# Kernel optimization log

Hardware: AMD Instinct MI355X
Metric: run time of the kernel (lower is better)

Reference implementation:

```python
import jax, jax.numpy as jnp
import numpy as np

N = 30000      # nodes
E = 480000     # edges (no self loops; GATConv adds them)
IN = 256       # in_features
OUT = 128      # out_features == per-head channels (concat=False)
H = 4          # heads
NEG_SLOPE = 0.2


def setup_inputs() -> dict:
    key = jax.random.key(0)
    k = jax.random.split(key, 6)
    x = jax.random.normal(k[0], (N, IN), dtype=jnp.float32)
    src = jax.random.randint(k[1], (E,), 0, N, dtype=jnp.int32)
    # guarantee no self loops (GATConv would strip them before re-adding)
    off = jax.random.randint(k[2], (E,), 1, N, dtype=jnp.int32)
    dst = (src + off) % N
    edge_index = jnp.stack([src, dst])  # [2, E]
    W = jax.random.normal(k[3], (IN, H * OUT), dtype=jnp.float32) / np.float32(np.sqrt(IN))
    att_src = jax.random.normal(k[4], (H, OUT), dtype=jnp.float32) / np.float32(np.sqrt(OUT))
    att_dst = jax.random.normal(k[5], (H, OUT), dtype=jnp.float32) / np.float32(np.sqrt(OUT))
    bias = jnp.zeros((OUT,), dtype=jnp.float32)
    return {"x": x, "edge_index": edge_index, "W": W,
            "att_src": att_src, "att_dst": att_dst, "bias": bias}


def reference(x, edge_index, W, att_src, att_dst, bias):
    n = x.shape[0]
    # dense projection -> per-head features [N, H, C]
    h = (x @ W).reshape(n, H, OUT)
    a_s = jnp.einsum('nhc,hc->nh', h, att_src)  # [N, H]
    a_d = jnp.einsum('nhc,hc->nh', h, att_dst)  # [N, H]
    # add self loops (GATConv default add_self_loops=True)
    loop = jnp.arange(n, dtype=edge_index.dtype)
    src = jnp.concatenate([edge_index[0], loop])  # [Et]
    dst = jnp.concatenate([edge_index[1], loop])  # [Et]
    # per-edge attention logits + LeakyReLU
    alpha = jax.nn.leaky_relu(a_s[src] + a_d[dst], NEG_SLOPE)  # [Et, H]
    # segment softmax over incoming edges of each dst node
    amax = jax.ops.segment_max(alpha, dst, num_segments=n)      # [N, H]
    ex = jnp.exp(alpha - amax[dst])
    denom = jax.ops.segment_sum(ex, dst, num_segments=n)        # [N, H]
    w = ex / denom[dst]                                          # [Et, H]
    # gather source features, weight, scatter-add to dst
    msg = h[src] * w[:, :, None]                                 # [Et, H, C]
    out = jax.ops.segment_sum(msg, dst, num_segments=n)          # [N, H, C]
    # concat=False -> mean over heads, then bias, then module's tanh
    out = out.mean(axis=1) + bias                                # [N, C]
    return jnp.tanh(out)
```

## Files before the change

### kernel.cpp

```cpp
#include <hip/hip_runtime.h>
#include <math.h>

#define IN_F   256
#define OUT_F  128
#define HEADS  4
#define HD     (HEADS * OUT_F)
#define K2     1024
#define NEG    0.2f
#define CAP    64

typedef __attribute__((ext_vector_type(8))) short short8;
typedef __attribute__((ext_vector_type(4))) float f32x4;
typedef __attribute__((ext_vector_type(2))) float f32x2;

typedef __attribute__((address_space(1))) const void* gp_t;
typedef __attribute__((address_space(3))) void* lp_t;

static __device__ __forceinline__ ushort f2bf(float f) {
    union { float f; unsigned u; } v; v.f = f;
    unsigned r = (v.u + 0x7FFFu + ((v.u >> 16) & 1u)) >> 16;
    return (ushort)r;
}
static __device__ __forceinline__ float bflo(unsigned u) {
    union { unsigned u; float f; } v; v.u = u << 16; return v.f;
}
static __device__ __forceinline__ float bfhi(unsigned u) {
    union { unsigned u; float f; } v; v.u = u & 0xFFFF0000u; return v.f;
}

#define PKFMA(D, A, B) asm("v_pk_fma_f32 %0, %1, %2, %0" : "+v"(D) : "v"(A), "v"(B))

__global__ __launch_bounds__(256) void prep1(const float* __restrict__ W,
                                             const float* __restrict__ att_src,
                                             const float* __restrict__ att_dst,
                                             ushort* __restrict__ WT2,
                                             float* __restrict__ va_s,
                                             float* __restrict__ va_d,
                                             int* __restrict__ cursor,
                                             int n_nodes) {
    const int b = blockIdx.x;
    const int tid = threadIdx.x;
    if (b < 512) {
        int idx = b * 256 + tid;
        int cout = idx >> 10, kk = idx & 1023;
        int h = kk >> 8, c = kk & 255;
        WT2[idx] = f2bf(W[(size_t)c * HD + h * OUT_F + cout]);
    } else if (b < 768) {
        const int lane = tid & 63;
        const int p = (b - 512) * 4 + (tid >> 6);
        const int h = p >> 8;
        const int k = p & 255;
        const float* wr = W + (size_t)k * HD + h * OUT_F;
        float w0 = wr[lane], w1 = wr[lane + 64];
        float s0 = att_src[h * OUT_F + lane], s1 = att_src[h * OUT_F + lane + 64];
        float d0 = att_dst[h * OUT_F + lane], d1 = att_dst[h * OUT_F + lane + 64];
        float ss = w0 * s0 + w1 * s1;
        float sd = w0 * d0 + w1 * d1;
#pragma unroll
        for (int off = 32; off > 0; off >>= 1) {
            ss += __shfl_xor(ss, off, 64);
            sd += __shfl_xor(sd, off, 64);
        }
        if (lane == 0) { va_s[p] = ss; va_d[p] = sd; }
    } else {
        int i = (b - 768) * 256 + tid;
        if (i < n_nodes) cursor[i] = 0;
    }
}

__global__ __launch_bounds__(256) void prep2(const float* __restrict__ X,
                                             const float* __restrict__ va_s,
                                             const float* __restrict__ va_d,
                                             const int* __restrict__ src,
                                             const int* __restrict__ dst,
                                             ushort* __restrict__ Xb,
                                             float* __restrict__ a_s,
                                             float* __restrict__ a_d,
                                             int* __restrict__ cursor,
                                             int* __restrict__ table,
                                             int n_nodes, int n_edges, int nebk) {
    const int b = blockIdx.x;
    const int tid = threadIdx.x;
    if (b < nebk) {
        int e = b * 256 + tid;
        if (e < n_edges) {
            int d = dst[e];
            int r = atomicAdd(&cursor[d], 1);
            if (r < CAP) table[(size_t)d * CAP + r] = src[e];
        }
        return;
    }
    const int lane = tid & 63;
    const int node = (b - nebk) * 4 + (tid >> 6);
    if (node >= n_nodes) return;
    float4 v = *(const float4*)(X + (size_t)node * IN_F + lane * 4);
    ushort4 o; o.x = f2bf(v.x); o.y = f2bf(v.y); o.z = f2bf(v.z); o.w = f2bf(v.w);
    *(ushort4*)(Xb + (size_t)node * IN_F + lane * 4) = o;

    float ps[HEADS], pd[HEADS];
#pragma unroll
    for (int hd = 0; hd < HEADS; ++hd) {
        float4 s4 = *(const float4*)(va_s + hd * IN_F + lane * 4);
        float4 d4 = *(const float4*)(va_d + hd * IN_F + lane * 4);
        ps[hd] = v.x * s4.x + v.y * s4.y + v.z * s4.z + v.w * s4.w;
        pd[hd] = v.x * d4.x + v.y * d4.y + v.z * d4.z + v.w * d4.w;
    }
#pragma unroll
    for (int off = 32; off > 0; off >>= 1) {
#pragma unroll
        for (int hd = 0; hd < HEADS; ++hd) {
            ps[hd] += __shfl_xor(ps[hd], off, 64);
            pd[hd] += __shfl_xor(pd[hd], off, 64);
        }
    }
    if (lane == 0) {
        float4 s4 = make_float4(ps[0], ps[1], ps[2], ps[3]);
        float4 d4 = make_float4(pd[0], pd[1], pd[2], pd[3]);
        *(float4*)(a_s + node * 4) = s4;
        *(float4*)(a_d + node * 4) = d4;
    }
}

#define EDGE(E8)                                                            \
    {                                                                       \
        uint u = *(const uint*)(cons + (E8) * 256);                         \
        float4 wA = *(const float4*)(wp + (E8) * 8);                        \
        float4 wB = *(const float4*)(wp + (E8) * 8 + 4);                    \
        f32x2 f = {bflo(u), bfhi(u)};                                       \
        f32x2 w0p = {wA.x, wA.y}, w1p = {wA.z, wA.w};                       \
        f32x2 w2p = {wB.x, wB.y}, w3p = {wB.z, wB.w};                       \
        PKFMA(ah[0], f, w0p); PKFMA(ah[1], f, w1p);                         \
        PKFMA(ah[2], f, w2p); PKFMA(ah[3], f, w3p);                         \
    }

#define ISSUE(EB, DST)                                                      \
    {                                                                       \
        asm volatile("s_waitcnt lgkmcnt(0)" ::: "memory");                  \
        int ea_ = __shfl(sreg, (EB) + (lane >> 4), 64);                     \
        int eb_ = __shfl(sreg, (EB) + 4 + (lane >> 4), 64);                 \
        __builtin_amdgcn_global_load_lds((gp_t)(xb16 + (size_t)ea_ * 256),  \
                                         (lp_t)(DST), 16, 0, 0);            \
        __builtin_amdgcn_global_load_lds((gp_t)(xb16 + (size_t)eb_ * 256),  \
                                         (lp_t)((DST) + 1024), 16, 0, 0);   \
    }

__global__ __launch_bounds__(256) void gat_agg(const ushort* __restrict__ Xb,
                                               const float* __restrict__ a_s,
                                               const float* __restrict__ a_d,
                                               const int* __restrict__ cursor,
                                               const int* __restrict__ table,
                                               ushort* __restrict__ Zb,
                                               int n_nodes) {
    __shared__ ushort xst[4][2][8][128];
    __shared__ float wse[4][CAP][8];
    const int lane = threadIdx.x & 63;
    const int wid  = threadIdx.x >> 6;
    const int n = blockIdx.x * 2 + (wid >> 1);
    const int half = wid & 1;
    if (n >= n_nodes) return;
    int deg = cursor[n]; if (deg > CAP) deg = CAP;
    const int* row = table + (size_t)n * CAP;
    const bool act = lane < deg;
    int sreg = act ? row[lane] : n;

    const ushort* xb16 = Xb + half * 128 + (lane & 15) * 8;
    uint uself = *(const uint*)(Xb + (size_t)n * IN_F + half * 128 + lane * 2);

    const int ntiles = (deg + 7) >> 3;
    if (ntiles > 0) ISSUE(0, (char*)&xst[wid][0][0][0]);

    const float4 ad4 = *(const float4*)(a_d + n * 4);
    const float4 as4 = *(const float4*)(a_s + n * 4);
    const float ad[4] = {ad4.x, ad4.y, ad4.z, ad4.w};
    float aself[4];
    {
        const float asn[4] = {as4.x, as4.y, as4.z, as4.w};
#pragma unroll
        for (int hd = 0; hd < 4; ++hd) {
            float al0 = asn[hd] + ad[hd];
            aself[hd] = al0 > 0.f ? al0 : NEG * al0;
        }
    }
    float al[4];
    {
        float4 av = *(const float4*)(a_s + (size_t)sreg * 4);
        const float as_[4] = {av.x, av.y, av.z, av.w};
#pragma unroll
        for (int hd = 0; hd < 4; ++hd) {
            float a = as_[hd] + ad[hd];
            a = a > 0.f ? a : NEG * a;
            al[hd] = act ? a : -1e30f;
        }
    }
    float m[4];
#pragma unroll
    for (int hd = 0; hd < 4; ++hd) m[hd] = al[hd];
#pragma unroll
    for (int off = 32; off > 0; off >>= 1)
#pragma unroll
        for (int hd = 0; hd < 4; ++hd)
            m[hd] = fmaxf(m[hd], __shfl_xor(m[hd], off, 64));
#pragma unroll
    for (int hd = 0; hd < 4; ++hd) m[hd] = fmaxf(m[hd], aself[hd]);

    float w[4], den[4];
#pragma unroll
    for (int hd = 0; hd < 4; ++hd) {
        w[hd] = act ? __expf(al[hd] - m[hd]) : 0.f;
        den[hd] = w[hd];
    }
#pragma unroll
    for (int off = 32; off > 0; off >>= 1)
#pragma unroll
        for (int hd = 0; hd < 4; ++hd)
            den[hd] += __shfl_xor(den[hd], off, 64);

    float es[4], rdv[4];
#pragma unroll
    for (int hd = 0; hd < 4; ++hd) {
        es[hd] = __expf(aself[hd] - m[hd]);
        rdv[hd] = 1.f / (den[hd] + es[hd]);
    }

    *(float4*)&wse[wid][lane][0] = make_float4(w[0], w[0], w[1], w[1]);
    *(float4*)&wse[wid][lane][4] = make_float4(w[2], w[2], w[3], w[3]);

    f32x2 ah[4];
    {
        f32x2 s = {bflo(uself), bfhi(uself)};
#pragma unroll
        for (int hd = 0; hd < 4; ++hd) {
            f32x2 eh = {es[hd], es[hd]};
            ah[hd] = s * eh;
        }
    }
#pragma unroll 1
    for (int t = 0; t < ntiles; ++t) {
        if (t + 1 < ntiles) {
            ISSUE((t + 1) * 8, (char*)&xst[wid][(t + 1) & 1][0][0]);
            asm volatile("s_waitcnt vmcnt(2)" ::: "memory");
        } else {
            asm volatile("s_waitcnt vmcnt(0)" ::: "memory");
        }
        const char* cons = (const char*)&xst[wid][t & 1][0][0] + lane * 4;
        const float* wp = &wse[wid][t * 8][0];
        EDGE(0); EDGE(1); EDGE(2); EDGE(3);
        EDGE(4); EDGE(5); EDGE(6); EDGE(7);
    }

    ushort* zr = Zb + (size_t)n * K2 + half * 128 + lane * 2;
#pragma unroll
    for (int hd = 0; hd < 4; ++hd) {
        f32x2 r2 = {rdv[hd], rdv[hd]};
        f32x2 z = ah[hd] * r2;
        ushort2 zz; zz.x = f2bf(z.x); zz.y = f2bf(z.y);
        *(ushort2*)(zr + hd * 256) = zz;
    }
}

#define GBM 32
#define GBN 128
#define GBK 64

__global__ __launch_bounds__(256) void gemm2(const ushort* __restrict__ Zb,
                                             const ushort* __restrict__ WT2,
                                             const float* __restrict__ bias,
                                             float* __restrict__ out,
                                             int n_nodes) {
    __shared__ ushort As[2][GBM][GBK];
    __shared__ ushort Bs[2][GBN][GBK];
    const int tid = threadIdx.x;
    const int m0 = blockIdx.y * GBM;
    const int wave = tid >> 6, lane = tid & 63;
    const int wm = (wave & 1) * 16, wn = (wave >> 1) * 64;
    const int l15 = lane & 15, quad = lane >> 4;

    const int rr8 = lane >> 3;
    const int cg  = (lane & 7) ^ rr8;
    const ushort* gA0 = Zb + (size_t)(m0 + wave * 8 + rr8) * K2 + cg * 8;
    const ushort* gB0 = WT2 + (size_t)(wave * 32 + rr8) * K2 + cg * 8;
    const ushort* gB1 = gB0 + 8 * K2;
    const ushort* gB2 = gB0 + 16 * K2;
    const ushort* gB3 = gB0 + 24 * K2;

#define STAGE(T, B)                                                          \
    {                                                                        \
        const int ko_ = (T) * GBK;                                           \
        __builtin_amdgcn_global_load_lds((gp_t)(gA0 + ko_),                  \
            (lp_t)&As[B][wave * 8][0], 16, 0, 0);                            \
        __builtin_amdgcn_global_load_lds((gp_t)(gB0 + ko_),                  \
            (lp_t)&Bs[B][wave * 32][0], 16, 0, 0);                           \
        __builtin_amdgcn_global_load_lds((gp_t)(gB1 + ko_),                  \
            (lp_t)&Bs[B][wave * 32 + 8][0], 16, 0, 0);                       \
        __builtin_amdgcn_global_load_lds((gp_t)(gB2 + ko_),                  \
            (lp_t)&Bs[B][wave * 32 + 16][0], 16, 0, 0);                      \
        __builtin_amdgcn_global_load_lds((gp_t)(gB3 + ko_),                  \
            (lp_t)&Bs[B][wave * 32 + 24][0], 16, 0, 0);                      \
    }

    f32x4 acc[4];
#pragma unroll
    for (int j = 0; j < 4; ++j) acc[j] = (f32x4){0.f, 0.f, 0.f, 0.f};

    const int NT = K2 / GBK;
    STAGE(0, 0);
#pragma unroll 1
    for (int t = 0; t < NT; ++t) {
        const int b = t & 1;
        if (t + 1 < NT) {
            STAGE(t + 1, b ^ 1);
            asm volatile("s_waitcnt vmcnt(5)" ::: "memory");
        } else {
            asm volatile("s_waitcnt vmcnt(0)" ::: "memory");
        }
        asm volatile("s_barrier" ::: "memory");

#pragma unroll
        for (int tt = 0; tt < 2; ++tt) {
            const int sl = ((tt * 4 + quad) ^ (l15 & 7)) * 8;
            short8 af = *(const short8*)&As[b][wm + l15][sl];
            short8 bf_[4];
#pragma unroll
            for (int fn = 0; fn < 4; ++fn)
                bf_[fn] = *(const short8*)&Bs[b][wn + fn * 16 + l15][sl];
#pragma unroll
            for (int fn = 0; fn < 4; ++fn)
                acc[fn] = __builtin_amdgcn_mfma_f32_16x16x32_bf16(
                    af, bf_[fn], acc[fn], 0, 0, 0);
        }
        asm volatile("s_barrier" ::: "memory");
    }

    float bcol[4];
#pragma unroll
    for (int fn = 0; fn < 4; ++fn) bcol[fn] = bias[wn + fn * 16 + l15];

    int gmb = m0 + wm + quad * 4;
#pragma unroll
    for (int reg = 0; reg < 4; ++reg) {
        int gm = gmb + reg;
        if (gm < n_nodes) {
#pragma unroll
            for (int fn = 0; fn < 4; ++fn) {
                float o = tanhf(0.25f * acc[fn][reg] + bcol[fn]);
                out[(size_t)gm * OUT_F + wn + fn * 16 + l15] = o;
            }
        }
    }
}

extern "C" void kernel_launch(void* const* d_in, const int* in_sizes, int n_in,
                              void* d_out, int out_size, void* d_ws, size_t ws_size,
                              hipStream_t stream) {
    const float* x       = (const float*)d_in[0];
    const int*   ei      = (const int*)d_in[1];
    const float* W       = (const float*)d_in[2];
    const float* att_src = (const float*)d_in[3];
    const float* att_dst = (const float*)d_in[4];
    const float* bias    = (const float*)d_in[5];
    float* out = (float*)d_out;

    const int n_nodes = in_sizes[0] / IN_F;
    const int n_edges = in_sizes[1] / 2;
    const int* src = ei;
    const int* dst = ei + n_edges;

    char* ws = (char*)d_ws;
    size_t off = 0;
    auto alloc = [&](size_t bytes) -> void* {
        void* p = ws + off;
        off = (off + bytes + 255) & ~(size_t)255;
        return p;
    };
    ushort* Xb     = (ushort*)alloc((size_t)n_nodes * IN_F * sizeof(ushort));
    ushort* Zb     = (ushort*)alloc((size_t)n_nodes * K2 * sizeof(ushort));
    ushort* WT2    = (ushort*)alloc((size_t)OUT_F * K2 * sizeof(ushort));
    float*  va_s   = (float*)alloc((size_t)HEADS * IN_F * sizeof(float));
    float*  va_d   = (float*)alloc((size_t)HEADS * IN_F * sizeof(float));
    float*  a_s    = (float*)alloc((size_t)n_nodes * HEADS * sizeof(float));
    float*  a_d    = (float*)alloc((size_t)n_nodes * HEADS * sizeof(float));
    int*    cursor = (int*)alloc((size_t)n_nodes * sizeof(int));
    int*    table  = (int*)alloc((size_t)n_nodes * CAP * sizeof(int));
    (void)ws_size; (void)n_in; (void)out_size;

    const int czb  = (n_nodes + 255) / 256;
    const int nebk = (n_edges + 255) / 256;

    prep1<<<768 + czb, 256, 0, stream>>>(W, att_src, att_dst, WT2, va_s, va_d,
                                         cursor, n_nodes);
    prep2<<<nebk + (n_nodes + 3) / 4, 256, 0, stream>>>(x, va_s, va_d, src, dst,
                                                        Xb, a_s, a_d, cursor, table,
                                                        n_nodes, n_edges, nebk);
    gat_agg<<<(n_nodes + 1) / 2, 256, 0, stream>>>(Xb, a_s, a_d, cursor, table,
                                                   Zb, n_nodes);

    dim3 ggrid(1, (n_nodes + GBM - 1) / GBM);
    gemm2<<<ggrid, 256, 0, stream>>>(Zb, WT2, bias, out, n_nodes);
}
```

Before: 204.8 us.

## Fuse neighbor aggregation and output GEMM into one kernel via LDS Z tile

Merges the gat_agg and gemm2 kernels into one, so each block of 32 nodes aggregates its neighbor features into a swizzled LDS tile and then runs the bf16 MFMA projection straight from LDS. This drops the global round trip of the N x 1024 bf16 Z intermediate and one kernel launch. Each wave now handles a full 256-wide row for 8 nodes serially instead of a half row for one node, which cuts parallelism and raises LDS use (64KB Z tile plus staging). Both effects may lower occupancy and latency hiding during the irregular gather phase.

```diff
diff --git a/kernel.cpp b/kernel.cpp
--- a/kernel.cpp
+++ b/kernel.cpp
@@ -8,6 +8,9 @@
 #define K2     1024
 #define NEG    0.2f
 #define CAP    64
+#define GBN    128
+#define GBK    64
+#define NTK    (K2 / GBK)
 
 typedef __attribute__((ext_vector_type(8))) short short8;
 typedef __attribute__((ext_vector_type(4))) float f32x4;
@@ -123,193 +126,214 @@
 
 #define EDGE(E8)                                                            \
     {                                                                       \
-        uint u = *(const uint*)(cons + (E8) * 256);                         \
+        uint2 uu = *(const uint2*)(cons + (E8) * 512);                      \
         float4 wA = *(const float4*)(wp + (E8) * 8);                        \
         float4 wB = *(const float4*)(wp + (E8) * 8 + 4);                    \
-        f32x2 f = {bflo(u), bfhi(u)};                                       \
+        f32x2 f01 = {bflo(uu.x), bfhi(uu.x)};                               \
+        f32x2 f23 = {bflo(uu.y), bfhi(uu.y)};                               \
         f32x2 w0p = {wA.x, wA.y}, w1p = {wA.z, wA.w};                       \
         f32x2 w2p = {wB.x, wB.y}, w3p = {wB.z, wB.w};                       \
-        PKFMA(ah[0], f, w0p); PKFMA(ah[1], f, w1p);                         \
-        PKFMA(ah[2], f, w2p); PKFMA(ah[3], f, w3p);                         \
+        PKFMA(a01[0], f01, w0p); PKFMA(a23[0], f23, w0p);                   \
+        PKFMA(a01[1], f01, w1p); PKFMA(a23[1], f23, w1p);                   \
+        PKFMA(a01[2], f01, w2p); PKFMA(a23[2], f23, w2p);                   \
+        PKFMA(a01[3], f01, w3p); PKFMA(a23[3], f23, w3p);                   \
     }
 
 #define ISSUE(EB, DST)                                                      \
     {                                                                       \
         asm volatile("s_waitcnt lgkmcnt(0)" ::: "memory");                  \
-        int ea_ = __shfl(sreg, (EB) + (lane >> 4), 64);                     \
-        int eb_ = __shfl(sreg, (EB) + 4 + (lane >> 4), 64);                 \
-        __builtin_amdgcn_global_load_lds((gp_t)(xb16 + (size_t)ea_ * 256),  \
-                                         (lp_t)(DST), 16, 0, 0);            \
-        __builtin_amdgcn_global_load_lds((gp_t)(xb16 + (size_t)eb_ * 256),  \
-                                         (lp_t)((DST) + 1024), 16, 0, 0);   \
-    }
-
-__global__ __launch_bounds__(256) void gat_agg(const ushort* __restrict__ Xb,
-                                               const float* __restrict__ a_s,
-                                               const float* __restrict__ a_d,
-                                               const int* __restrict__ cursor,
-                                               const int* __restrict__ table,
-                                               ushort* __restrict__ Zb,
-                                               int n_nodes) {
-    __shared__ ushort xst[4][2][8][128];
+        int s0_ = __shfl(sreg, (EB) + 0, 64);                               \
+        int s1_ = __shfl(sreg, (EB) + 1, 64);                               \
+        int s2_ = __shfl(sreg, (EB) + 2, 64);                               \
+        int s3_ = __shfl(sreg, (EB) + 3, 64);                               \
+        int s4_ = __shfl(sreg, (EB) + 4, 64);                               \
+        int s5_ = __shfl(sreg, (EB) + 5, 64);                               \
+        int s6_ = __shfl(sreg, (EB) + 6, 64);                               \
+        int s7_ = __shfl(sreg, (EB) + 7, 64);                               \
+        int sa_ = (lane & 32) ? s1_ : s0_;                                  \
+        int sb_ = (lane & 32) ? s3_ : s2_;                                  \
+        int sc_ = (lane & 32) ? s5_ : s4_;                                  \
+        int sd_ = (lane & 32) ? s7_ : s6_;                                  \
+        __builtin_amdgcn_global_load_lds((gp_t)(xb16 + (size_t)sa_ * 256),  \
+                                         (lp_t)((DST) + 0 * 1024), 16, 0, 0);\
+        __builtin_amdgcn_global_load_lds((gp_t)(xb16 + (size_t)sb_ * 256),  \
+                                         (lp_t)((DST) + 1 * 1024), 16, 0, 0);\
+        __builtin_amdgcn_global_load_lds((gp_t)(xb16 + (size_t)sc_ * 256),  \
+                                         (lp_t)((DST) + 2 * 1024), 16, 0, 0);\
+        __builtin_amdgcn_global_load_lds((gp_t)(xb16 + (size_t)sd_ * 256),  \
+                                         (lp_t)((DST) + 3 * 1024), 16, 0, 0);\
+    }
+
+#define STAGEB(T, B)                                                         \
+    {                                                                        \
+        const int ko_ = (T) * GBK;                                           \
+        __builtin_amdgcn_global_load_lds((gp_t)(gB0 + ko_),                  \
+            (lp_t)&u.Bs[B][wid * 32][0], 16, 0, 0);                          \
+        __builtin_amdgcn_global_load_lds((gp_t)(gB1 + ko_),                  \
+            (lp_t)&u.Bs[B][wid * 32 + 8][0], 16, 0, 0);                      \
+        __builtin_amdgcn_global_load_lds((gp_t)(gB2 + ko_),                  \
+            (lp_t)&u.Bs[B][wid * 32 + 16][0], 16, 0, 0);                     \
+        __builtin_amdgcn_global_load_lds((gp_t)(gB3 + ko_),                  \
+            (lp_t)&u.Bs[B][wid * 32 + 24][0], 16, 0, 0);                     \
+    }
+
+union staging_u {
+    ushort xst[4][2][8][256];
+    ushort Bs[2][GBN][GBK];
+};
+
+__global__ __launch_bounds__(256) void aggemm(const ushort* __restrict__ Xb,
+                                              const float* __restrict__ a_s,
+                                              const float* __restrict__ a_d,
+                                              const int* __restrict__ cursor,
+                                              const int* __restrict__ table,
+                                              const ushort* __restrict__ WT2,
+                                              const float* __restrict__ bias,
+                                              float* __restrict__ out,
+                                              int n_nodes) {
+    __shared__ ushort Zs[32][K2];
+    __shared__ union staging_u u;
     __shared__ float wse[4][CAP][8];
+
     const int lane = threadIdx.x & 63;
     const int wid  = threadIdx.x >> 6;
-    const int n = blockIdx.x * 2 + (wid >> 1);
-    const int half = wid & 1;
-    if (n >= n_nodes) return;
-    int deg = cursor[n]; if (deg > CAP) deg = CAP;
-    const int* row = table + (size_t)n * CAP;
-    const bool act = lane < deg;
-    int sreg = act ? row[lane] : n;
-
-    const ushort* xb16 = Xb + half * 128 + (lane & 15) * 8;
-    uint uself = *(const uint*)(Xb + (size_t)n * IN_F + half * 128 + lane * 2);
-
-    const int ntiles = (deg + 7) >> 3;
-    if (ntiles > 0) ISSUE(0, (char*)&xst[wid][0][0][0]);
-
-    const float4 ad4 = *(const float4*)(a_d + n * 4);
-    const float4 as4 = *(const float4*)(a_s + n * 4);
-    const float ad[4] = {ad4.x, ad4.y, ad4.z, ad4.w};
-    float aself[4];
-    {
-        const float asn[4] = {as4.x, as4.y, as4.z, as4.w};
+    const int m0 = blockIdx.x * 32;
+
+    const ushort* xb16 = Xb + (lane & 31) * 8;
+    const uint2* xb2 = (const uint2*)Xb;
+    char* xb0 = (char*)&u.xst[wid][0][0][0];
+    char* xb1 = (char*)&u.xst[wid][1][0][0];
+
+    for (int i = 0; i < 8; ++i) {
+        const int slot = wid * 8 + i;
+        const int n = m0 + slot;
+        if (n >= n_nodes) break;
+        int deg = cursor[n]; if (deg > CAP) deg = CAP;
+        const int* row = table + (size_t)n * CAP;
+        const bool act = lane < deg;
+        int sreg = act ? row[lane] : n;
+        uint2 uself = xb2[(size_t)n * 64 + lane];
+
+        const int ntiles = (deg + 7) >> 3;
+        if (ntiles > 0) ISSUE(0, xb0);
+
+        const float4 ad4 = *(const float4*)(a_d + n * 4);
+        const float4 as4 = *(const float4*)(a_s + n * 4);
+        const float ad[4] = {ad4.x, ad4.y, ad4.z, ad4.w};
+        float aself[4];
+        {
+            const float asn[4] = {as4.x, as4.y, as4.z, as4.w};
+#pragma unroll
+            for (int hd = 0; hd < 4; ++hd) {
+                float al0 = asn[hd] + ad[hd];
+                aself[hd] = al0 > 0.f ? al0 : NEG * al0;
+            }
+        }
+        float al[4];
+        {
+            float4 av = *(const float4*)(a_s + (size_t)sreg * 4);
+            const float as_[4] = {av.x, av.y, av.z, av.w};
+#pragma unroll
+            for (int hd = 0; hd < 4; ++hd) {
+                float a = as_[hd] + ad[hd];
+                a = a > 0.f ? a : NEG * a;
+                al[hd] = act ? a : -1e30f;
+            }
+        }
+        float m[4];
+#pragma unroll
+        for (int hd = 0; hd < 4; ++hd) m[hd] = al[hd];
+#pragma unroll
+        for (int off = 32; off > 0; off >>= 1)
+#pragma unroll
+            for (int hd = 0; hd < 4; ++hd)
+                m[hd] = fmaxf(m[hd], __shfl_xor(m[hd], off, 64));
+#pragma unroll
+        for (int hd = 0; hd < 4; ++hd) m[hd] = fmaxf(m[hd], aself[hd]);
+
+        float w[4], den[4];
 #pragma unroll
         for (int hd = 0; hd < 4; ++hd) {
-            float al0 = asn[hd] + ad[hd];
-            aself[hd] = al0 > 0.f ? al0 : NEG * al0;
-        }
-    }
-    float al[4];
-    {
-        float4 av = *(const float4*)(a_s + (size_t)sreg * 4);
-        const float as_[4] = {av.x, av.y, av.z, av.w};
+            w[hd] = act ? __expf(al[hd] - m[hd]) : 0.f;
+            den[hd] = w[hd];
+        }
+#pragma unroll
+        for (int off = 32; off > 0; off >>= 1)
+#pragma unroll
+            for (int hd = 0; hd < 4; ++hd)
+                den[hd] += __shfl_xor(den[hd], off, 64);
+
+        float es[4], rdv[4];
 #pragma unroll
         for (int hd = 0; hd < 4; ++hd) {
-            float a = as_[hd] + ad[hd];
-            a = a > 0.f ? a : NEG * a;
-            al[hd] = act ? a : -1e30f;
-        }
-    }
-    float m[4];
-#pragma unroll
-    for (int hd = 0; hd < 4; ++hd) m[hd] = al[hd];
-#pragma unroll
-    for (int off = 32; off > 0; off >>= 1)
-#pragma unroll
-        for (int hd = 0; hd < 4; ++hd)
-            m[hd] = fmaxf(m[hd], __shfl_xor(m[hd], off, 64));
-#pragma unroll
-    for (int hd = 0; hd < 4; ++hd) m[hd] = fmaxf(m[hd], aself[hd]);
-
-    float w[4], den[4];
-#pragma unroll
-    for (int hd = 0; hd < 4; ++hd) {
-        w[hd] = act ? __expf(al[hd] - m[hd]) : 0.f;
-        den[hd] = w[hd];
-    }
-#pragma unroll
-    for (int off = 32; off > 0; off >>= 1)
-#pragma unroll
-        for (int hd = 0; hd < 4; ++hd)
-            den[hd] += __shfl_xor(den[hd], off, 64);
-
-    float es[4], rdv[4];
-#pragma unroll
-    for (int hd = 0; hd < 4; ++hd) {
-        es[hd] = __expf(aself[hd] - m[hd]);
-        rdv[hd] = 1.f / (den[hd] + es[hd]);
-    }
-
-    *(float4*)&wse[wid][lane][0] = make_float4(w[0], w[0], w[1], w[1]);
-    *(float4*)&wse[wid][lane][4] = make_float4(w[2], w[2], w[3], w[3]);
-
-    f32x2 ah[4];
-    {
-        f32x2 s = {bflo(uself), bfhi(uself)};
+            es[hd] = __expf(aself[hd] - m[hd]);
+            rdv[hd] = 1.f / (den[hd] + es[hd]);
+        }
+
+        asm volatile("s_waitcnt lgkmcnt(0)" ::: "memory");
+        *(float4*)&wse[wid][lane][0] = make_float4(w[0], w[0], w[1], w[1]);
+        *(float4*)&wse[wid][lane][4] = make_float4(w[2], w[2], w[3], w[3]);
+
+        f32x2 a01[4], a23[4];
+        {
+            f32x2 s01 = {bflo(uself.x), bfhi(uself.x)};
+            f32x2 s23 = {bflo(uself.y), bfhi(uself.y)};
+#pragma unroll
+            for (int hd = 0; hd < 4; ++hd) {
+                f32x2 eh = {es[hd], es[hd]};
+                a01[hd] = s01 * eh;
+                a23[hd] = s23 * eh;
+            }
+        }
+#pragma unroll 1
+        for (int t = 0; t < ntiles; ++t) {
+            if (t + 1 < ntiles) {
+                ISSUE((t + 1) * 8, ((t + 1) & 1) ? xb1 : xb0);
+                asm volatile("s_waitcnt vmcnt(4)" ::: "memory");
+            } else {
+                asm volatile("s_waitcnt vmcnt(0)" ::: "memory");
+            }
+            const char* cons = ((t & 1) ? xb1 : xb0) + lane * 8;
+            const float* wp = &wse[wid][t * 8][0];
+            EDGE(0); EDGE(1); EDGE(2); EDGE(3);
+            EDGE(4); EDGE(5); EDGE(6); EDGE(7);
+        }
+
+        char* zrow = (char*)&Zs[slot][0];
+        const int swz = (slot & 7) << 4;
 #pragma unroll
         for (int hd = 0; hd < 4; ++hd) {
-            f32x2 eh = {es[hd], es[hd]};
-            ah[hd] = s * eh;
-        }
-    }
-#pragma unroll 1
-    for (int t = 0; t < ntiles; ++t) {
-        if (t + 1 < ntiles) {
-            ISSUE((t + 1) * 8, (char*)&xst[wid][(t + 1) & 1][0][0]);
-            asm volatile("s_waitcnt vmcnt(2)" ::: "memory");
-        } else {
-            asm volatile("s_waitcnt vmcnt(0)" ::: "memory");
-        }
-        const char* cons = (const char*)&xst[wid][t & 1][0][0] + lane * 4;
-        const float* wp = &wse[wid][t * 8][0];
-        EDGE(0); EDGE(1); EDGE(2); EDGE(3);
-        EDGE(4); EDGE(5); EDGE(6); EDGE(7);
-    }
-
-    ushort* zr = Zb + (size_t)n * K2 + half * 128 + lane * 2;
-#pragma unroll
-    for (int hd = 0; hd < 4; ++hd) {
-        f32x2 r2 = {rdv[hd], rdv[hd]};
-        f32x2 z = ah[hd] * r2;
-        ushort2 zz; zz.x = f2bf(z.x); zz.y = f2bf(z.y);
-        *(ushort2*)(zr + hd * 256) = zz;
-    }
-}
-
-#define GBM 32
-#define GBN 128
-#define GBK 64
-
-__global__ __launch_bounds__(256) void gemm2(const ushort* __restrict__ Zb,
-                                             const ushort* __restrict__ WT2,
-                                             const float* __restrict__ bias,
-                                             float* __restrict__ out,
-                                             int n_nodes) {
-    __shared__ ushort As[2][GBM][GBK];
-    __shared__ ushort Bs[2][GBN][GBK];
-    const int tid = threadIdx.x;
-    const int m0 = blockIdx.y * GBM;
-    const int wave = tid >> 6, lane = tid & 63;
-    const int wm = (wave & 1) * 16, wn = (wave >> 1) * 64;
+            f32x2 r2 = {rdv[hd], rdv[hd]};
+            f32x2 z01 = a01[hd] * r2;
+            f32x2 z23 = a23[hd] * r2;
+            ushort4 z;
+            z.x = f2bf(z01.x); z.y = f2bf(z01.y);
+            z.z = f2bf(z23.x); z.w = f2bf(z23.y);
+            *(ushort4*)(zrow + ((hd * 512 + lane * 8) ^ swz)) = z;
+        }
+    }
+    __syncthreads();
+
+    const int wm = (wid & 1) * 16, wn = (wid >> 1) * 64;
     const int l15 = lane & 15, quad = lane >> 4;
-
     const int rr8 = lane >> 3;
-    const int cg  = (lane & 7) ^ rr8;
-    const ushort* gA0 = Zb + (size_t)(m0 + wave * 8 + rr8) * K2 + cg * 8;
-    const ushort* gB0 = WT2 + (size_t)(wave * 32 + rr8) * K2 + cg * 8;
+    const int cgx = (lane & 7) ^ rr8;
+    const ushort* gB0 = WT2 + (size_t)(wid * 32 + rr8) * K2 + cgx * 8;
     const ushort* gB1 = gB0 + 8 * K2;
     const ushort* gB2 = gB0 + 16 * K2;
     const ushort* gB3 = gB0 + 24 * K2;
 
-#define STAGE(T, B)                                                          \
-    {                                                                        \
-        const int ko_ = (T) * GBK;                                           \
-        __builtin_amdgcn_global_load_lds((gp_t)(gA0 + ko_),                  \
-            (lp_t)&As[B][wave * 8][0], 16, 0, 0);                            \
-        __builtin_amdgcn_global_load_lds((gp_t)(gB0 + ko_),                  \
-            (lp_t)&Bs[B][wave * 32][0], 16, 0, 0);                           \
-        __builtin_amdgcn_global_load_lds((gp_t)(gB1 + ko_),                  \
-            (lp_t)&Bs[B][wave * 32 + 8][0], 16, 0, 0);                       \
-        __builtin_amdgcn_global_load_lds((gp_t)(gB2 + ko_),                  \
-            (lp_t)&Bs[B][wave * 32 + 16][0], 16, 0, 0);                      \
-        __builtin_amdgcn_global_load_lds((gp_t)(gB3 + ko_),                  \
-            (lp_t)&Bs[B][wave * 32 + 24][0], 16, 0, 0);                      \
-    }
-
     f32x4 acc[4];
 #pragma unroll
     for (int j = 0; j < 4; ++j) acc[j] = (f32x4){0.f, 0.f, 0.f, 0.f};
 
-    const int NT = K2 / GBK;
-    STAGE(0, 0);
+    STAGEB(0, 0);
 #pragma unroll 1
-    for (int t = 0; t < NT; ++t) {
+    for (int t = 0; t < NTK; ++t) {
         const int b = t & 1;
-        if (t + 1 < NT) {
-            STAGE(t + 1, b ^ 1);
-            asm volatile("s_waitcnt vmcnt(5)" ::: "memory");
+        if (t + 1 < NTK) {
+            STAGEB(t + 1, b ^ 1);
+            asm volatile("s_waitcnt vmcnt(4)" ::: "memory");
         } else {
             asm volatile("s_waitcnt vmcnt(0)" ::: "memory");
         }
@@ -318,11 +342,12 @@
 #pragma unroll
         for (int tt = 0; tt < 2; ++tt) {
             const int sl = ((tt * 4 + quad) ^ (l15 & 7)) * 8;
-            short8 af = *(const short8*)&As[b][wm + l15][sl];
             short8 bf_[4];
 #pragma unroll
             for (int fn = 0; fn < 4; ++fn)
-                bf_[fn] = *(const short8*)&Bs[b][wn + fn * 16 + l15][sl];
+                bf_[fn] = *(const short8*)&u.Bs[b][wn + fn * 16 + l15][sl];
+            const int byteA = (t * 128 + tt * 64 + quad * 16) ^ ((l15 & 7) << 4);
+            short8 af = *(const short8*)((const char*)&Zs[wm + l15][0] + byteA);
 #pragma unroll
             for (int fn = 0; fn < 4; ++fn)
                 acc[fn] = __builtin_amdgcn_mfma_f32_16x16x32_bf16(
@@ -373,7 +398,6 @@
         return p;
     };
     ushort* Xb     = (ushort*)alloc((size_t)n_nodes * IN_F * sizeof(ushort));
-    ushort* Zb     = (ushort*)alloc((size_t)n_nodes * K2 * sizeof(ushort));
     ushort* WT2    = (ushort*)alloc((size_t)OUT_F * K2 * sizeof(ushort));
     float*  va_s   = (float*)alloc((size_t)HEADS * IN_F * sizeof(float));
     float*  va_d   = (float*)alloc((size_t)HEADS * IN_F * sizeof(float));
@@ -391,9 +415,6 @@
     prep2<<<nebk + (n_nodes + 3) / 4, 256, 0, stream>>>(x, va_s, va_d, src, dst,
                                                         Xb, a_s, a_d, cursor, table,
                                                         n_nodes, n_edges, nebk);
-    gat_agg<<<(n_nodes + 1) / 2, 256, 0, stream>>>(Xb, a_s, a_d, cursor, table,
-                                                   Zb, n_nodes);
-
-    dim3 ggrid(1, (n_nodes + GBM - 1) / GBM);
-    gemm2<<<ggrid, 256, 0, stream>>>(Zb, WT2, bias, out, n_nodes);
-}
+    aggemm<<<(n_nodes + 31) / 32, 256, 0, stream>>>(Xb, a_s, a_d, cursor, table,
+                                                    WT2, bias, out, n_nodes);
+}
```

Result: slower. 286.7 us (+40.0%).

## Process one node per wave with 4-channel lanes and triple-buffered gathers

Applied to the files above, without the earlier changes.

The aggregation kernel now assigns each destination node to a single wave covering all 256 input channels, with each lane handling four channels instead of two. This halves redundant per-node work: the softmax, the edge table read and the weight computation are no longer duplicated across two half-waves. Neighbor feature gathers move to 4-edge tiles with a three-deep LDS ring buffer so that two tiles are in flight while one is consumed. In exchange each lane carries twice as many accumulator registers, and each node's edge loop runs serially over all channels in one wave.

```diff
diff --git a/kernel.cpp b/kernel.cpp
--- a/kernel.cpp
+++ b/kernel.cpp
@@ -123,24 +123,27 @@
 
 #define EDGE(E8)                                                            \
     {                                                                       \
-        uint u = *(const uint*)(cons + (E8) * 256);                         \
+        uint2 uu = *(const uint2*)(cons + (E8) * 512);                      \
         float4 wA = *(const float4*)(wp + (E8) * 8);                        \
         float4 wB = *(const float4*)(wp + (E8) * 8 + 4);                    \
-        f32x2 f = {bflo(u), bfhi(u)};                                       \
+        f32x2 f01 = {bflo(uu.x), bfhi(uu.x)};                               \
+        f32x2 f23 = {bflo(uu.y), bfhi(uu.y)};                               \
         f32x2 w0p = {wA.x, wA.y}, w1p = {wA.z, wA.w};                       \
         f32x2 w2p = {wB.x, wB.y}, w3p = {wB.z, wB.w};                       \
-        PKFMA(ah[0], f, w0p); PKFMA(ah[1], f, w1p);                         \
-        PKFMA(ah[2], f, w2p); PKFMA(ah[3], f, w3p);                         \
-    }
-
-#define ISSUE(EB, DST)                                                      \
+        PKFMA(a01[0], f01, w0p); PKFMA(a23[0], f23, w0p);                   \
+        PKFMA(a01[1], f01, w1p); PKFMA(a23[1], f23, w1p);                   \
+        PKFMA(a01[2], f01, w2p); PKFMA(a23[2], f23, w2p);                   \
+        PKFMA(a01[3], f01, w3p); PKFMA(a23[3], f23, w3p);                   \
+    }
+
+#define ISSUE4(EB, DST)                                                     \
     {                                                                       \
         asm volatile("s_waitcnt lgkmcnt(0)" ::: "memory");                  \
-        int ea_ = __shfl(sreg, (EB) + (lane >> 4), 64);                     \
-        int eb_ = __shfl(sreg, (EB) + 4 + (lane >> 4), 64);                 \
-        __builtin_amdgcn_global_load_lds((gp_t)(xb16 + (size_t)ea_ * 256),  \
+        int sa_ = __shfl(sreg, (EB) + ((lane >> 5) & 1), 64);               \
+        int sb_ = __shfl(sreg, (EB) + 2 + ((lane >> 5) & 1), 64);           \
+        __builtin_amdgcn_global_load_lds((gp_t)(xb16 + (size_t)sa_ * 256),  \
                                          (lp_t)(DST), 16, 0, 0);            \
-        __builtin_amdgcn_global_load_lds((gp_t)(xb16 + (size_t)eb_ * 256),  \
+        __builtin_amdgcn_global_load_lds((gp_t)(xb16 + (size_t)sb_ * 256),  \
                                          (lp_t)((DST) + 1024), 16, 0, 0);   \
     }
 
@@ -151,23 +154,28 @@
                                                const int* __restrict__ table,
                                                ushort* __restrict__ Zb,
                                                int n_nodes) {
-    __shared__ ushort xst[4][2][8][128];
+    __shared__ ushort xst[4][3][4][256];
     __shared__ float wse[4][CAP][8];
     const int lane = threadIdx.x & 63;
     const int wid  = threadIdx.x >> 6;
-    const int n = blockIdx.x * 2 + (wid >> 1);
-    const int half = wid & 1;
+    const int n = blockIdx.x * 4 + wid;
     if (n >= n_nodes) return;
     int deg = cursor[n]; if (deg > CAP) deg = CAP;
     const int* row = table + (size_t)n * CAP;
     const bool act = lane < deg;
     int sreg = act ? row[lane] : n;
 
-    const ushort* xb16 = Xb + half * 128 + (lane & 15) * 8;
-    uint uself = *(const uint*)(Xb + (size_t)n * IN_F + half * 128 + lane * 2);
-
-    const int ntiles = (deg + 7) >> 3;
-    if (ntiles > 0) ISSUE(0, (char*)&xst[wid][0][0][0]);
+    const ushort* xb16 = Xb + (lane & 31) * 8;
+    const uint2* xb2 = (const uint2*)Xb;
+    uint2 uself = xb2[(size_t)n * 64 + lane];
+
+    char* cA = (char*)&xst[wid][0][0][0];
+    char* cB = (char*)&xst[wid][1][0][0];
+    char* cC = (char*)&xst[wid][2][0][0];
+
+    const int ntiles = (deg + 3) >> 2;
+    if (ntiles > 0) ISSUE4(0, cA);
+    if (ntiles > 1) ISSUE4(4, cB);
 
     const float4 ad4 = *(const float4*)(a_d + n * 4);
     const float4 as4 = *(const float4*)(a_s + n * 4);
@@ -225,36 +233,44 @@
     *(float4*)&wse[wid][lane][0] = make_float4(w[0], w[0], w[1], w[1]);
     *(float4*)&wse[wid][lane][4] = make_float4(w[2], w[2], w[3], w[3]);
 
-    f32x2 ah[4];
+    f32x2 a01[4], a23[4];
     {
-        f32x2 s = {bflo(uself), bfhi(uself)};
+        f32x2 s01 = {bflo(uself.x), bfhi(uself.x)};
+        f32x2 s23 = {bflo(uself.y), bfhi(uself.y)};
 #pragma unroll
         for (int hd = 0; hd < 4; ++hd) {
             f32x2 eh = {es[hd], es[hd]};
-            ah[hd] = s * eh;
+            a01[hd] = s01 * eh;
+            a23[hd] = s23 * eh;
         }
     }
 #pragma unroll 1
     for (int t = 0; t < ntiles; ++t) {
-        if (t + 1 < ntiles) {
-            ISSUE((t + 1) * 8, (char*)&xst[wid][(t + 1) & 1][0][0]);
+        const int rem = ntiles - t;
+        if (rem > 2) {
+            ISSUE4((t + 2) * 4, cC);
+            asm volatile("s_waitcnt vmcnt(4)" ::: "memory");
+        } else if (rem == 2) {
             asm volatile("s_waitcnt vmcnt(2)" ::: "memory");
         } else {
             asm volatile("s_waitcnt vmcnt(0)" ::: "memory");
         }
-        const char* cons = (const char*)&xst[wid][t & 1][0][0] + lane * 4;
-        const float* wp = &wse[wid][t * 8][0];
+        const char* cons = cA + lane * 8;
+        const float* wp = &wse[wid][t * 4][0];
         EDGE(0); EDGE(1); EDGE(2); EDGE(3);
-        EDGE(4); EDGE(5); EDGE(6); EDGE(7);
-    }
-
-    ushort* zr = Zb + (size_t)n * K2 + half * 128 + lane * 2;
+        char* tmp = cA; cA = cB; cB = cC; cC = tmp;
+    }
+
+    ushort* zr = Zb + (size_t)n * K2;
 #pragma unroll
     for (int hd = 0; hd < 4; ++hd) {
         f32x2 r2 = {rdv[hd], rdv[hd]};
-        f32x2 z = ah[hd] * r2;
-        ushort2 zz; zz.x = f2bf(z.x); zz.y = f2bf(z.y);
-        *(ushort2*)(zr + hd * 256) = zz;
+        f32x2 z01 = a01[hd] * r2;
+        f32x2 z23 = a23[hd] * r2;
+        ushort4 z;
+        z.x = f2bf(z01.x); z.y = f2bf(z01.y);
+        z.z = f2bf(z23.x); z.w = f2bf(z23.y);
+        *(ushort4*)(zr + hd * 256 + lane * 4) = z;
     }
 }
 
@@ -391,7 +407,7 @@
     prep2<<<nebk + (n_nodes + 3) / 4, 256, 0, stream>>>(x, va_s, va_d, src, dst,
                                                         Xb, a_s, a_d, cursor, table,
                                                         n_nodes, n_edges, nebk);
-    gat_agg<<<(n_nodes + 1) / 2, 256, 0, stream>>>(Xb, a_s, a_d, cursor, table,
+    gat_agg<<<(n_nodes + 3) / 4, 256, 0, stream>>>(Xb, a_s, a_d, cursor, table,
                                                    Zb, n_nodes);
 
     dim3 ggrid(1, (n_nodes + GBM - 1) / GBM);
```

New measurement: 197.5 us. -3.6%, faster.
